# Kernel tuning notes

Measured on AMD Instinct MI355X. Metric: run time of the kernel, lower is better.

Reference implementation:

```python
import jax, jax.numpy as jnp
import numpy as np

TOP_K = 2


def setup_inputs() -> dict:
    key = jax.random.key(0)
    ks = jax.random.split(key, 6)
    B, S, D, F, E = 4, 2048, 1024, 4096, 8
    sd = 1.0 / np.sqrt(D)
    sf = 1.0 / np.sqrt(F)
    return {
        "x": jax.random.normal(ks[0], (B, S, D), dtype=jnp.float32),
        "gate_w": jax.random.normal(ks[1], (D, E), dtype=jnp.float32) * sd,
        "w1": jax.random.normal(ks[2], (E, D, F), dtype=jnp.float32) * sd,
        "b1": jax.random.normal(ks[3], (E, F), dtype=jnp.float32) * 0.01,
        "w2": jax.random.normal(ks[4], (E, F, D), dtype=jnp.float32) * sf,
        "b2": jax.random.normal(ks[5], (E, D), dtype=jnp.float32) * 0.01,
    }


def reference(x, gate_w, w1, b1, w2, b2):
    B, S, D = x.shape
    E = gate_w.shape[1]
    xf = x.reshape(-1, D)                        # [T, D], T = B*S
    T = xf.shape[0]

    # Gating: top-k logits, softmax over the selected k (in fp32, as in torch)
    logits = xf @ gate_w                         # [T, E]
    top_vals, top_idx = jax.lax.top_k(logits, TOP_K)            # [T, K]
    wts = jax.nn.softmax(top_vals.astype(jnp.float32), axis=-1).astype(x.dtype)

    # Dense combine weights: combine[t, e] = sum_k wts[t,k] * [top_idx[t,k]==e]
    rows = jnp.arange(T)[:, None]
    combine = jnp.zeros((T, E), dtype=x.dtype).at[rows, top_idx].add(wts)

    # Expert FFNs (dropout is identity in eval; torch GELU default = exact erf)
    out = jnp.zeros_like(xf)
    for e in range(E):
        h = jax.nn.gelu(xf @ w1[e] + b1[e], approximate=False)  # [T, F]
        out = out + combine[:, e:e + 1] * (h @ w2[e] + b2[e])
    return out.reshape(B, S, D)
```

## Files before the change

kernel.cpp:

```cpp
#include <hip/hip_runtime.h>


#define T_TOK 8192
#define D_DIM 1024
#define F_DIM 4096
#define E_NUM 8
#define BM 128
#define BN 128
#define BK 32
#define MAX_TILES (T_TOK * 2 / BM + E_NUM)

typedef float f32x4 __attribute__((ext_vector_type(4)));
typedef short bf16x8 __attribute__((ext_vector_type(8)));

__device__ __forceinline__ unsigned short f2bf(float f) {
  union { float f; unsigned u; } v; v.f = f;
  unsigned r = v.u + 0x7FFFu + ((v.u >> 16) & 1u);
  return (unsigned short)(r >> 16);
}

__device__ __forceinline__ void async_cp16(const unsigned short* g, unsigned short* l) {
  __builtin_amdgcn_global_load_lds((__attribute__((address_space(1))) void*)g,
                                   (__attribute__((address_space(3))) void*)l,
                                   16, 0, 0);
}


__global__ void cast_x_kernel(const float* __restrict__ src,
                              unsigned short* __restrict__ dst, int n4) {
  int i = blockIdx.x * blockDim.x + threadIdx.x;
  if (i >= n4) return;
  float4 v = ((const float4*)src)[i];
  ushort4 o;
  o.x = f2bf(v.x); o.y = f2bf(v.y); o.z = f2bf(v.z); o.w = f2bf(v.w);
  ((ushort4*)dst)[i] = o;
}

__global__ void transpose_cast_kernel(const float* __restrict__ src,
                                      unsigned short* __restrict__ dst,
                                      int R, int C) {
  __shared__ float tile[64][65];
  int e = blockIdx.z;
  src += (size_t)e * R * C;
  dst += (size_t)e * R * C;
  int c0 = blockIdx.x * 64;
  int r0 = blockIdx.y * 64;
  int tc = threadIdx.x & 63, tr = threadIdx.x >> 6;
#pragma unroll
  for (int i = 0; i < 16; ++i) {
    int r = tr + i * 4;
    tile[r][tc] = src[(size_t)(r0 + r) * C + c0 + tc];
  }
  __syncthreads();
#pragma unroll
  for (int i = 0; i < 16; ++i) {
    int c = tr + i * 4;
    dst[(size_t)(c0 + c) * R + r0 + tc] = f2bf(tile[tc][c]);
  }
}

__global__ __launch_bounds__(256) void gate_kernel(
    const float* __restrict__ x, const float* __restrict__ gw,
    float* __restrict__ topk_w, int* __restrict__ topk_e) {
  int t = (blockIdx.x * 256 + threadIdx.x) >> 6;
  int lane = threadIdx.x & 63;
  const float* xr = x + (size_t)t * D_DIM;
  float acc[8];
#pragma unroll
  for (int e = 0; e < 8; ++e) acc[e] = 0.f;
  for (int j = 0; j < D_DIM / 64; ++j) {
    int d = lane + 64 * j;
    float xv = xr[d];
    float4 g0 = ((const float4*)(gw + (size_t)d * 8))[0];
    float4 g1 = ((const float4*)(gw + (size_t)d * 8))[1];
    acc[0] += xv * g0.x; acc[1] += xv * g0.y;
    acc[2] += xv * g0.z; acc[3] += xv * g0.w;
    acc[4] += xv * g1.x; acc[5] += xv * g1.y;
    acc[6] += xv * g1.z; acc[7] += xv * g1.w;
  }
#pragma unroll
  for (int off = 32; off > 0; off >>= 1) {
#pragma unroll
    for (int e = 0; e < 8; ++e) acc[e] += __shfl_xor(acc[e], off);
  }
  if (lane == 0) {
    int e0 = 0; float v0 = acc[0];
#pragma unroll
    for (int e = 1; e < 8; ++e)
      if (acc[e] > v0) { v0 = acc[e]; e0 = e; }
    int e1 = -1; float v1 = -1e30f;
#pragma unroll
    for (int e = 0; e < 8; ++e)
      if (e != e0 && acc[e] > v1) { v1 = acc[e]; e1 = e; }
    float ex = expf(v1 - v0);
    float inv = 1.f / (1.f + ex);
    topk_w[2 * t] = inv;
    topk_w[2 * t + 1] = ex * inv;
    topk_e[2 * t] = e0;
    topk_e[2 * t + 1] = e1;
  }
}

__global__ void scatter_kernel(const int* __restrict__ topk_e,
                               int* __restrict__ cnt, int* __restrict__ assign) {
  int idx = blockIdx.x * blockDim.x + threadIdx.x;
  int e = topk_e[idx];
  int pos = atomicAdd(&cnt[e], 1);
  assign[e * T_TOK + pos] = idx;
}

__global__ void tiles_kernel(const int* __restrict__ cnt,
                             int* __restrict__ ndesc, int4* __restrict__ desc) {
  if (threadIdx.x != 0) return;
  int nt = 0, hb = 0;
  for (int e = 0; e < E_NUM; ++e) {
    int c = cnt[e];
    for (int s = 0; s < c; s += BM) {
      int4 d;
      d.x = e; d.y = s; d.z = hb;
      d.w = (c - s < BM) ? (c - s) : BM;
      desc[nt++] = d;
    }
    hb += c;
  }
  *ndesc = nt;
}


__global__ __launch_bounds__(256) void gemm1_kernel(
    const unsigned short* __restrict__ xb, const unsigned short* __restrict__ w1t,
    const float* __restrict__ b1, const int* __restrict__ assign,
    const int* __restrict__ ndesc, const int4* __restrict__ desc,
    unsigned short* __restrict__ H) {
  int tileid = blockIdx.y;
  if (tileid >= *ndesc) return;
  int4 dc = desc[tileid];
  int e = dc.x, start = dc.y, hbase = dc.z, mcnt = dc.w;
  int n0 = blockIdx.x * BN;

  __shared__ __attribute__((aligned(16))) unsigned short As[BM * BK];
  __shared__ __attribute__((aligned(16))) unsigned short Bs[BN * BK];

  int tid = threadIdx.x, lane = tid & 63, wv = tid >> 6;

  const unsigned short* gA[2]; const unsigned short* gB[2];
  unsigned short* lA[2]; unsigned short* lB[2];
#pragma unroll
  for (int s = 0; s < 2; ++s) {
    int L = tid + s * 256;
    int row = L >> 2, cc = L & 3;
    int g = (cc - row) & 3;
    int rowc = row < mcnt ? row : (mcnt - 1);
    int a = assign[e * T_TOK + start + rowc];
    gA[s] = xb + (size_t)(a >> 1) * D_DIM + g * 8;
    gB[s] = w1t + (size_t)(e * F_DIM + n0 + row) * D_DIM + g * 8;
    lA[s] = As + (size_t)(s * 256 + wv * 64) * 8;
    lB[s] = Bs + (size_t)(s * 256 + wv * 64) * 8;
  }

  int kc = lane >> 4, r16 = lane & 15;
  int m_off = (wv & 1) * 64, n_off = (wv >> 1) * 64;
  int aoff[4], boff[4];
#pragma unroll
  for (int i = 0; i < 4; ++i) {
    int ra = m_off + i * 16 + r16;
    aoff[i] = ra * 32 + ((kc + ra) & 3) * 8;
    int rb = n_off + i * 16 + r16;
    boff[i] = rb * 32 + ((kc + rb) & 3) * 8;
  }

  f32x4 acc[4][4];
#pragma unroll
  for (int i = 0; i < 4; ++i)
#pragma unroll
    for (int j = 0; j < 4; ++j) acc[i][j] = (f32x4){0.f, 0.f, 0.f, 0.f};

  for (int kt = 0; kt < D_DIM / BK; ++kt) {
#pragma unroll
    for (int s = 0; s < 2; ++s) {
      async_cp16(gA[s], lA[s]);
      async_cp16(gB[s], lB[s]);
      gA[s] += BK; gB[s] += BK;
    }
    __syncthreads();
    bf16x8 af[4], bfr[4];
#pragma unroll
    for (int i = 0; i < 4; ++i) af[i] = *(const bf16x8*)(As + aoff[i]);
#pragma unroll
    for (int i = 0; i < 4; ++i) bfr[i] = *(const bf16x8*)(Bs + boff[i]);
#pragma unroll
    for (int i = 0; i < 4; ++i)
#pragma unroll
      for (int j = 0; j < 4; ++j)
        acc[i][j] = __builtin_amdgcn_mfma_f32_16x16x32_bf16(af[i], bfr[j], acc[i][j], 0, 0, 0);
    __syncthreads();
  }

  int col = lane & 15, rbase = (lane >> 4) * 4;
  float bias[4];
#pragma unroll
  for (int j = 0; j < 4; ++j) bias[j] = b1[e * F_DIM + n0 + n_off + j * 16 + col];
#pragma unroll
  for (int i = 0; i < 4; ++i) {
#pragma unroll
    for (int rg = 0; rg < 4; ++rg) {
      int r = m_off + i * 16 + rbase + rg;
      if (r < mcnt) {
        unsigned short* hrow = H + (size_t)(hbase + start + r) * F_DIM + n0 + n_off + col;
#pragma unroll
        for (int j = 0; j < 4; ++j) {
          float v = acc[i][j][rg] + bias[j];
          v = 0.5f * v * (1.0f + erff(v * 0.70710678118654752f));
          hrow[j * 16] = f2bf(v);
        }
      }
    }
  }
}

__global__ __launch_bounds__(256) void gemm2_kernel(
    const unsigned short* __restrict__ H, const unsigned short* __restrict__ w2t,
    const float* __restrict__ b2, const int* __restrict__ assign,
    const float* __restrict__ topk_w,
    const int* __restrict__ ndesc, const int4* __restrict__ desc,
    float* __restrict__ out) {
  int tileid = blockIdx.y;
  if (tileid >= *ndesc) return;
  int4 dc = desc[tileid];
  int e = dc.x, start = dc.y, hbase = dc.z, mcnt = dc.w;
  int n0 = blockIdx.x * BN;

  __shared__ __attribute__((aligned(16))) unsigned short As[BM * BK];
  __shared__ __attribute__((aligned(16))) unsigned short Bs[BN * BK];

  int tid = threadIdx.x, lane = tid & 63, wv = tid >> 6;

  const unsigned short* gA[2]; const unsigned short* gB[2];
  unsigned short* lA[2]; unsigned short* lB[2];
#pragma unroll
  for (int s = 0; s < 2; ++s) {
    int L = tid + s * 256;
    int row = L >> 2, cc = L & 3;
    int g = (cc - row) & 3;
    int rowc = row < mcnt ? row : (mcnt - 1);
    gA[s] = H + (size_t)(hbase + start + rowc) * F_DIM + g * 8;
    gB[s] = w2t + (size_t)(e * D_DIM + n0 + row) * F_DIM + g * 8;
    lA[s] = As + (size_t)(s * 256 + wv * 64) * 8;
    lB[s] = Bs + (size_t)(s * 256 + wv * 64) * 8;
  }

  int kc = lane >> 4, r16 = lane & 15;
  int m_off = (wv & 1) * 64, n_off = (wv >> 1) * 64;
  int aoff[4], boff[4];
#pragma unroll
  for (int i = 0; i < 4; ++i) {
    int ra = m_off + i * 16 + r16;
    aoff[i] = ra * 32 + ((kc + ra) & 3) * 8;
    int rb = n_off + i * 16 + r16;
    boff[i] = rb * 32 + ((kc + rb) & 3) * 8;
  }

  f32x4 acc[4][4];
#pragma unroll
  for (int i = 0; i < 4; ++i)
#pragma unroll
    for (int j = 0; j < 4; ++j) acc[i][j] = (f32x4){0.f, 0.f, 0.f, 0.f};

  for (int kt = 0; kt < F_DIM / BK; ++kt) {
#pragma unroll
    for (int s = 0; s < 2; ++s) {
      async_cp16(gA[s], lA[s]);
      async_cp16(gB[s], lB[s]);
      gA[s] += BK; gB[s] += BK;
    }
    __syncthreads();
    bf16x8 af[4], bfr[4];
#pragma unroll
    for (int i = 0; i < 4; ++i) af[i] = *(const bf16x8*)(As + aoff[i]);
#pragma unroll
    for (int i = 0; i < 4; ++i) bfr[i] = *(const bf16x8*)(Bs + boff[i]);
#pragma unroll
    for (int i = 0; i < 4; ++i)
#pragma unroll
      for (int j = 0; j < 4; ++j)
        acc[i][j] = __builtin_amdgcn_mfma_f32_16x16x32_bf16(af[i], bfr[j], acc[i][j], 0, 0, 0);
    __syncthreads();
  }

  int col = lane & 15, rbase = (lane >> 4) * 4;
  float bias[4];
#pragma unroll
  for (int j = 0; j < 4; ++j) bias[j] = b2[e * D_DIM + n0 + n_off + j * 16 + col];
#pragma unroll
  for (int i = 0; i < 4; ++i) {
#pragma unroll
    for (int rg = 0; rg < 4; ++rg) {
      int r = m_off + i * 16 + rbase + rg;
      if (r < mcnt) {
        int a = assign[e * T_TOK + start + r];
        float wt = topk_w[a];
        float* orow = out + (size_t)(a >> 1) * D_DIM + n0 + n_off + col;
#pragma unroll
        for (int j = 0; j < 4; ++j) {
          float v = acc[i][j][rg] + bias[j];
          atomicAdd(orow + j * 16, wt * v);
        }
      }
    }
  }
}


extern "C" void kernel_launch(void* const* d_in, const int* in_sizes, int n_in,
                              void* d_out, int out_size, void* d_ws, size_t ws_size,
                              hipStream_t stream) {
  const float* x      = (const float*)d_in[0];
  const float* gate_w = (const float*)d_in[1];
  const float* w1     = (const float*)d_in[2];
  const float* b1     = (const float*)d_in[3];
  const float* w2     = (const float*)d_in[4];
  const float* b2     = (const float*)d_in[5];
  float* out = (float*)d_out;

  char* ws = (char*)d_ws;
  size_t off = 0;
  auto alloc = [&](size_t bytes) {
    char* p = ws + off;
    off = (off + bytes + 255) & ~(size_t)255;
    return p;
  };
  unsigned short* xb   = (unsigned short*)alloc((size_t)T_TOK * D_DIM * 2);
  unsigned short* w1t  = (unsigned short*)alloc((size_t)E_NUM * D_DIM * F_DIM * 2);
  unsigned short* w2t  = (unsigned short*)alloc((size_t)E_NUM * D_DIM * F_DIM * 2);
  unsigned short* Hbuf = (unsigned short*)alloc((size_t)2 * T_TOK * F_DIM * 2);
  float* topk_w = (float*)alloc((size_t)2 * T_TOK * 4);
  int* topk_e   = (int*)alloc((size_t)2 * T_TOK * 4);
  int* assign   = (int*)alloc((size_t)E_NUM * T_TOK * 4);
  int* cnt      = (int*)alloc(64);
  int* ndesc    = (int*)alloc(64);
  int4* desc    = (int4*)alloc((size_t)MAX_TILES * 16);

  hipMemsetAsync(cnt, 0, 64, stream);
  hipMemsetAsync(out, 0, (size_t)out_size * 4, stream);

  cast_x_kernel<<<(T_TOK * D_DIM / 4 + 255) / 256, 256, 0, stream>>>(
      x, xb, T_TOK * D_DIM / 4);
  transpose_cast_kernel<<<dim3(F_DIM / 64, D_DIM / 64, E_NUM), 256, 0, stream>>>(
      w1, w1t, D_DIM, F_DIM);
  transpose_cast_kernel<<<dim3(D_DIM / 64, F_DIM / 64, E_NUM), 256, 0, stream>>>(
      w2, w2t, F_DIM, D_DIM);
  gate_kernel<<<T_TOK / 4, 256, 0, stream>>>(x, gate_w, topk_w, topk_e);
  scatter_kernel<<<2 * T_TOK / 256, 256, 0, stream>>>(topk_e, cnt, assign);
  tiles_kernel<<<1, 64, 0, stream>>>(cnt, ndesc, desc);
  gemm1_kernel<<<dim3(F_DIM / BN, MAX_TILES), 256, 0, stream>>>(
      xb, w1t, b1, assign, ndesc, desc, Hbuf);
  gemm2_kernel<<<dim3(D_DIM / BN, MAX_TILES), 256, 0, stream>>>(
      Hbuf, w2t, b2, assign, topk_w, ndesc, desc, out);
}
```

Baseline: 916.5 us.

## Double-buffer LDS tiles in expert GEMMs and vectorize weight transpose-cast

Both expert GEMM kernels now keep two LDS buffers and prefetch the K-tile two steps ahead with async global-to-LDS loads. Explicit vmcnt/lgkmcnt waits and raw barriers replace the two __syncthreads per iteration, so global loads can overlap the MFMA work. The weight transpose-cast kernel also switches to float4 loads and ushort4 stores with a padded tile. This doubles LDS use per block, and the hand-written waitcnt logic is fragile: it relies on the compiler not reordering memory operations, and tail iterations issue redundant clamped loads.

```diff
diff --git a/kernel.cpp b/kernel.cpp
--- a/kernel.cpp
+++ b/kernel.cpp
@@ -8,6 +8,8 @@
 #define BM 128
 #define BN 128
 #define BK 32
+#define NK1 (D_DIM / BK)
+#define NK2 (F_DIM / BK)
 #define MAX_TILES (T_TOK * 2 / BM + E_NUM)
 
 typedef float f32x4 __attribute__((ext_vector_type(4)));
@@ -24,6 +26,10 @@
                                    (__attribute__((address_space(3))) void*)l,
                                    16, 0, 0);
 }
+
+#define WAIT_VM4 asm volatile("s_waitcnt vmcnt(4)" ::: "memory")
+#define WAIT_LGKM0 asm volatile("s_waitcnt lgkmcnt(0)" ::: "memory")
+#define RAW_BARRIER asm volatile("s_barrier" ::: "memory")
 
 
 __global__ void cast_x_kernel(const float* __restrict__ src,
@@ -36,26 +42,34 @@
   ((ushort4*)dst)[i] = o;
 }
 
-__global__ void transpose_cast_kernel(const float* __restrict__ src,
-                                      unsigned short* __restrict__ dst,
-                                      int R, int C) {
-  __shared__ float tile[64][65];
+__global__ __launch_bounds__(256) void transpose_cast_kernel(
+    const float* __restrict__ src, unsigned short* __restrict__ dst,
+    int R, int C) {
+  __shared__ float tile[64][68];
   int e = blockIdx.z;
   src += (size_t)e * R * C;
   dst += (size_t)e * R * C;
   int c0 = blockIdx.x * 64;
   int r0 = blockIdx.y * 64;
-  int tc = threadIdx.x & 63, tr = threadIdx.x >> 6;
-#pragma unroll
-  for (int i = 0; i < 16; ++i) {
-    int r = tr + i * 4;
-    tile[r][tc] = src[(size_t)(r0 + r) * C + c0 + tc];
+  int t = threadIdx.x;
+  int cl = (t & 15) * 4, rl = t >> 4;
+#pragma unroll
+  for (int i = 0; i < 4; ++i) {
+    int r = rl + i * 16;
+    float4 v = *(const float4*)(src + (size_t)(r0 + r) * C + c0 + cl);
+    *(float4*)&tile[r][cl] = v;
   }
   __syncthreads();
-#pragma unroll
-  for (int i = 0; i < 16; ++i) {
-    int c = tr + i * 4;
-    dst[(size_t)(c0 + c) * R + r0 + tc] = f2bf(tile[tc][c]);
+  int rl2 = (t & 15) * 4, cl2 = t >> 4;
+#pragma unroll
+  for (int i = 0; i < 4; ++i) {
+    int c = cl2 + i * 16;
+    ushort4 o;
+    o.x = f2bf(tile[rl2 + 0][c]);
+    o.y = f2bf(tile[rl2 + 1][c]);
+    o.z = f2bf(tile[rl2 + 2][c]);
+    o.w = f2bf(tile[rl2 + 3][c]);
+    *(ushort4*)(dst + (size_t)(c0 + c) * R + r0 + rl2) = o;
   }
 }
 
@@ -138,13 +152,13 @@
   int e = dc.x, start = dc.y, hbase = dc.z, mcnt = dc.w;
   int n0 = blockIdx.x * BN;
 
-  __shared__ __attribute__((aligned(16))) unsigned short As[BM * BK];
-  __shared__ __attribute__((aligned(16))) unsigned short Bs[BN * BK];
+  __shared__ __attribute__((aligned(16))) unsigned short As[2][BM * BK];
+  __shared__ __attribute__((aligned(16))) unsigned short Bs[2][BN * BK];
 
   int tid = threadIdx.x, lane = tid & 63, wv = tid >> 6;
 
   const unsigned short* gA[2]; const unsigned short* gB[2];
-  unsigned short* lA[2]; unsigned short* lB[2];
+  int loff[2];
 #pragma unroll
   for (int s = 0; s < 2; ++s) {
     int L = tid + s * 256;
@@ -154,19 +168,18 @@
     int a = assign[e * T_TOK + start + rowc];
     gA[s] = xb + (size_t)(a >> 1) * D_DIM + g * 8;
     gB[s] = w1t + (size_t)(e * F_DIM + n0 + row) * D_DIM + g * 8;
-    lA[s] = As + (size_t)(s * 256 + wv * 64) * 8;
-    lB[s] = Bs + (size_t)(s * 256 + wv * 64) * 8;
-  }
-
-  int kc = lane >> 4, r16 = lane & 15;
+    loff[s] = (s * 256 + wv * 64) * 8;
+  }
+
+  int kc16 = lane >> 4, r16 = lane & 15;
   int m_off = (wv & 1) * 64, n_off = (wv >> 1) * 64;
   int aoff[4], boff[4];
 #pragma unroll
   for (int i = 0; i < 4; ++i) {
     int ra = m_off + i * 16 + r16;
-    aoff[i] = ra * 32 + ((kc + ra) & 3) * 8;
+    aoff[i] = ra * 32 + ((kc16 + ra) & 3) * 8;
     int rb = n_off + i * 16 + r16;
-    boff[i] = rb * 32 + ((kc + rb) & 3) * 8;
+    boff[i] = rb * 32 + ((kc16 + rb) & 3) * 8;
   }
 
   f32x4 acc[4][4];
@@ -175,26 +188,35 @@
 #pragma unroll
     for (int j = 0; j < 4; ++j) acc[i][j] = (f32x4){0.f, 0.f, 0.f, 0.f};
 
-  for (int kt = 0; kt < D_DIM / BK; ++kt) {
+  auto issue = [&](int t, int b) {
+    int kc = (t < NK1 ? t : NK1 - 1) * BK;
 #pragma unroll
     for (int s = 0; s < 2; ++s) {
-      async_cp16(gA[s], lA[s]);
-      async_cp16(gB[s], lB[s]);
-      gA[s] += BK; gB[s] += BK;
-    }
-    __syncthreads();
+      async_cp16(gA[s] + kc, &As[b][loff[s]]);
+      async_cp16(gB[s] + kc, &Bs[b][loff[s]]);
+    }
+  };
+  auto step = [&](int kt, int b) {
+    WAIT_VM4;
+    RAW_BARRIER;
     bf16x8 af[4], bfr[4];
 #pragma unroll
-    for (int i = 0; i < 4; ++i) af[i] = *(const bf16x8*)(As + aoff[i]);
-#pragma unroll
-    for (int i = 0; i < 4; ++i) bfr[i] = *(const bf16x8*)(Bs + boff[i]);
+    for (int i = 0; i < 4; ++i) af[i] = *(const bf16x8*)(&As[b][0] + aoff[i]);
+#pragma unroll
+    for (int i = 0; i < 4; ++i) bfr[i] = *(const bf16x8*)(&Bs[b][0] + boff[i]);
+    WAIT_LGKM0;
+    RAW_BARRIER;
+    issue(kt + 2, b);
 #pragma unroll
     for (int i = 0; i < 4; ++i)
 #pragma unroll
       for (int j = 0; j < 4; ++j)
         acc[i][j] = __builtin_amdgcn_mfma_f32_16x16x32_bf16(af[i], bfr[j], acc[i][j], 0, 0, 0);
-    __syncthreads();
-  }
+  };
+
+  issue(0, 0);
+  issue(1, 1);
+  for (int kt = 0; kt < NK1; kt += 2) { step(kt, 0); step(kt + 1, 1); }
 
   int col = lane & 15, rbase = (lane >> 4) * 4;
   float bias[4];
@@ -230,13 +252,13 @@
   int e = dc.x, start = dc.y, hbase = dc.z, mcnt = dc.w;
   int n0 = blockIdx.x * BN;
 
-  __shared__ __attribute__((aligned(16))) unsigned short As[BM * BK];
-  __shared__ __attribute__((aligned(16))) unsigned short Bs[BN * BK];
+  __shared__ __attribute__((aligned(16))) unsigned short As[2][BM * BK];
+  __shared__ __attribute__((aligned(16))) unsigned short Bs[2][BN * BK];
 
   int tid = threadIdx.x, lane = tid & 63, wv = tid >> 6;
 
   const unsigned short* gA[2]; const unsigned short* gB[2];
-  unsigned short* lA[2]; unsigned short* lB[2];
+  int loff[2];
 #pragma unroll
   for (int s = 0; s < 2; ++s) {
     int L = tid + s * 256;
@@ -245,19 +267,18 @@
     int rowc = row < mcnt ? row : (mcnt - 1);
     gA[s] = H + (size_t)(hbase + start + rowc) * F_DIM + g * 8;
     gB[s] = w2t + (size_t)(e * D_DIM + n0 + row) * F_DIM + g * 8;
-    lA[s] = As + (size_t)(s * 256 + wv * 64) * 8;
-    lB[s] = Bs + (size_t)(s * 256 + wv * 64) * 8;
-  }
-
-  int kc = lane >> 4, r16 = lane & 15;
+    loff[s] = (s * 256 + wv * 64) * 8;
+  }
+
+  int kc16 = lane >> 4, r16 = lane & 15;
   int m_off = (wv & 1) * 64, n_off = (wv >> 1) * 64;
   int aoff[4], boff[4];
 #pragma unroll
   for (int i = 0; i < 4; ++i) {
     int ra = m_off + i * 16 + r16;
-    aoff[i] = ra * 32 + ((kc + ra) & 3) * 8;
+    aoff[i] = ra * 32 + ((kc16 + ra) & 3) * 8;
     int rb = n_off + i * 16 + r16;
-    boff[i] = rb * 32 + ((kc + rb) & 3) * 8;
+    boff[i] = rb * 32 + ((kc16 + rb) & 3) * 8;
   }
 
   f32x4 acc[4][4];
@@ -266,26 +287,35 @@
 #pragma unroll
     for (int j = 0; j < 4; ++j) acc[i][j] = (f32x4){0.f, 0.f, 0.f, 0.f};
 
-  for (int kt = 0; kt < F_DIM / BK; ++kt) {
+  auto issue = [&](int t, int b) {
+    int kc = (t < NK2 ? t : NK2 - 1) * BK;
 #pragma unroll
     for (int s = 0; s < 2; ++s) {
-      async_cp16(gA[s], lA[s]);
-      async_cp16(gB[s], lB[s]);
-      gA[s] += BK; gB[s] += BK;
-    }
-    __syncthreads();
+      async_cp16(gA[s] + kc, &As[b][loff[s]]);
+      async_cp16(gB[s] + kc, &Bs[b][loff[s]]);
+    }
+  };
+  auto step = [&](int kt, int b) {
+    WAIT_VM4;
+    RAW_BARRIER;
     bf16x8 af[4], bfr[4];
 #pragma unroll
-    for (int i = 0; i < 4; ++i) af[i] = *(const bf16x8*)(As + aoff[i]);
-#pragma unroll
-    for (int i = 0; i < 4; ++i) bfr[i] = *(const bf16x8*)(Bs + boff[i]);
+    for (int i = 0; i < 4; ++i) af[i] = *(const bf16x8*)(&As[b][0] + aoff[i]);
+#pragma unroll
+    for (int i = 0; i < 4; ++i) bfr[i] = *(const bf16x8*)(&Bs[b][0] + boff[i]);
+    WAIT_LGKM0;
+    RAW_BARRIER;
+    issue(kt + 2, b);
 #pragma unroll
     for (int i = 0; i < 4; ++i)
 #pragma unroll
       for (int j = 0; j < 4; ++j)
         acc[i][j] = __builtin_amdgcn_mfma_f32_16x16x32_bf16(af[i], bfr[j], acc[i][j], 0, 0, 0);
-    __syncthreads();
-  }
+  };
+
+  issue(0, 0);
+  issue(1, 1);
+  for (int kt = 0; kt < NK2; kt += 2) { step(kt, 0); step(kt + 1, 1); }
 
   int col = lane & 15, rbase = (lane >> 4) * 4;
   float bias[4];
```

Result: no change. 918.7 us (+0.2%).
